# Optimization experiments

Hardware: AMD Instinct MI355X
Metric: run time of the kernel (lower is better)

The kernel has to match this reference:

```python
import jax, jax.numpy as jnp
import numpy as np

N = 256
MAX_LENGTH = 1024
BATCH = 32768


def _transition(n):
    # HiPPO-LegS transition matrices (float64 numpy, matches torch module)
    q = np.arange(n, dtype=np.float64)
    col, row = np.meshgrid(q, q)
    r = 2 * q + 1
    M = -(np.where(row >= col, r, 0) - np.diag(q))
    T = np.sqrt(np.diag(2 * q + 1))
    A = T @ M @ np.linalg.inv(T)
    B = np.diag(T)  # squeezed (N,)
    return A, B


def _build_stacked(n, max_length):
    # Bilinear (Tustin) discretization at every timescale t=1..max_length.
    A, B = _transition(n)
    ts = np.arange(1, max_length + 1, dtype=np.float64)  # (L,)
    At = A[None] / ts[:, None, None]                     # (L,N,N)
    Bt = B[None] / ts[:, None]                           # (L,N)
    I = np.eye(n)
    lhs = I[None] - At / 2                               # (L,N,N), lower triangular
    A_stacked = np.linalg.solve(lhs, I[None] + At / 2)   # (L,N,N)
    B_stacked = np.linalg.solve(lhs, Bt[..., None])[..., 0]  # (L,N)
    return A_stacked.astype(np.float32), B_stacked.astype(np.float32)


def setup_inputs() -> dict:
    key = jax.random.key(0)
    k1, k2 = jax.random.split(key)
    A_np, B_np = _build_stacked(N, MAX_LENGTH)
    return {
        "c": jax.random.normal(k1, (BATCH, N), dtype=jnp.float32),
        "f": jax.random.normal(k2, (BATCH, 1), dtype=jnp.float32),
        "A_stacked": jnp.asarray(A_np),  # (L, N, N) buffer
        "B_stacked": jnp.asarray(B_np),  # (L, N) buffer
        "t": 512,
    }


def reference(c, f, A_stacked, B_stacked, t):
    # F.linear(c, A) == c @ A.T ; then scaled add of new value f
    A = A_stacked[t]            # (N, N)
    b = B_stacked[t]            # (N,)
    return c @ A.T + b * f      # (BATCH, N)
```

## Files before the change

### kernel.cpp

```cpp
#include <hip/hip_runtime.h>
#include <cstdint>
#include <cstddef>

typedef _Float16 half8 __attribute__((ext_vector_type(8)));
typedef float f32x4 __attribute__((ext_vector_type(4)));

static constexpr int kN  = 256;
static constexpr int kKS = 8;
static constexpr size_t kABytes = (size_t)kN * kN * 2;

__global__ __launch_bounds__(256) void hippo_prep(
    const float* __restrict__ A_stacked, const int* __restrict__ tptr,
    _Float16* __restrict__ a16)
{
    const int t = tptr[0];
    const float* __restrict__ A = A_stacked + (size_t)t * kN * kN;
    const int tid = blockIdx.x * 256 + threadIdx.x;
    const int nt = tid >> 9;
    const int ks = (tid >> 6) & 7;
    const int l  = tid & 63;
    const int row = nt * 16 + (l & 15);
    const int k0  = ks * 32 + ((l >> 4) << 3);
    const float* __restrict__ src = A + row * kN + k0;
    f32x4 v0 = *(const f32x4*)(src);
    f32x4 v1 = *(const f32x4*)(src + 4);
    half8 h;
    h[0] = (_Float16)v0[0]; h[1] = (_Float16)v0[1];
    h[2] = (_Float16)v0[2]; h[3] = (_Float16)v0[3];
    h[4] = (_Float16)v1[0]; h[5] = (_Float16)v1[1];
    h[6] = (_Float16)v1[2]; h[7] = (_Float16)v1[3];
    ((half8*)a16)[tid] = h;
}

__global__ __launch_bounds__(512, 2) void hippo_gemm(
    const float* __restrict__ c, const float* __restrict__ f,
    const float* __restrict__ Bst, const int* __restrict__ tptr,
    const _Float16* __restrict__ a16, float* __restrict__ out)
{
    extern __shared__ char lds_raw[];

    const int tid  = threadIdx.x;
    const int l    = tid & 63;
    const int wid  = tid >> 6;
    const int wm   = wid & 3;
    const int wn   = wid >> 2;
    const int lo16 = l & 15;
    const int hi4  = l >> 4;
    const int m0   = blockIdx.x * 128 + wm * 16;
    const int m1   = m0 + 64;
    const int ntb  = wn * 8;

    const float* __restrict__ cp0 = c + (size_t)(m0 + lo16) * kN + (hi4 << 3);
    f32x4 cv0[kKS], cv1[kKS];
    #pragma unroll
    for (int ks = 0; ks < kKS; ++ks) {
        cv0[ks] = *(const f32x4*)(cp0 + ks * 32);
        cv1[ks] = *(const f32x4*)(cp0 + ks * 32 + 4);
    }

    #pragma unroll
    for (int i = 0; i < 16; ++i) {
        const size_t off = (size_t)(i * 8 + wid) * 1024 + (size_t)l * 16;
        __builtin_amdgcn_global_load_lds(
            (const __attribute__((address_space(1))) void*)((const char*)a16 + off),
            (__attribute__((address_space(3))) void*)(lds_raw + off),
            16, 0, 0);
    }

    const int t = tptr[0];
    const float* __restrict__ brow = Bst + (size_t)t * kN + wn * 128;
    float bvs[8];
    #pragma unroll
    for (int nt = 0; nt < 8; ++nt) bvs[nt] = brow[nt * 16 + lo16];
    float fv0[4], fv1[4];
    #pragma unroll
    for (int r = 0; r < 4; ++r) {
        fv0[r] = f[m0 + (hi4 << 2) + r];
        fv1[r] = f[m1 + (hi4 << 2) + r];
    }

    __syncthreads();

    const float* __restrict__ cp1 = c + (size_t)(m1 + lo16) * kN + (hi4 << 3);
    f32x4 dv0[kKS], dv1[kKS];
    #pragma unroll
    for (int ks = 0; ks < kKS; ++ks) {
        dv0[ks] = *(const f32x4*)(cp1 + ks * 32);
        dv1[ks] = *(const f32x4*)(cp1 + ks * 32 + 4);
    }

    half8 af[kKS];
    #pragma unroll
    for (int ks = 0; ks < kKS; ++ks) {
        af[ks][0] = (_Float16)cv0[ks][0]; af[ks][1] = (_Float16)cv0[ks][1];
        af[ks][2] = (_Float16)cv0[ks][2]; af[ks][3] = (_Float16)cv0[ks][3];
        af[ks][4] = (_Float16)cv1[ks][0]; af[ks][5] = (_Float16)cv1[ks][1];
        af[ks][6] = (_Float16)cv1[ks][2]; af[ks][7] = (_Float16)cv1[ks][3];
    }
    const half8* __restrict__ Bs = (const half8*)lds_raw;
    f32x4 acc[8];
    #pragma unroll
    for (int i = 0; i < 8; ++i) acc[i] = (f32x4){0.f, 0.f, 0.f, 0.f};
    #pragma unroll
    for (int ks = 0; ks < kKS; ++ks) {
        #pragma unroll
        for (int nt = 0; nt < 8; ++nt) {
            half8 bf = Bs[((ntb + nt) * kKS + ks) * 64 + l];
            acc[nt] = __builtin_amdgcn_mfma_f32_16x16x32_f16(af[ks], bf, acc[nt], 0, 0, 0);
        }
    }
    float* __restrict__ ob0 = out + (size_t)(m0 + (hi4 << 2)) * kN + wn * 128 + lo16;
    #pragma unroll
    for (int nt = 0; nt < 8; ++nt) {
        #pragma unroll
        for (int r = 0; r < 4; ++r)
            ob0[(size_t)r * kN + nt * 16] = acc[nt][r] + bvs[nt] * fv0[r];
    }

    half8 ag[kKS];
    #pragma unroll
    for (int ks = 0; ks < kKS; ++ks) {
        ag[ks][0] = (_Float16)dv0[ks][0]; ag[ks][1] = (_Float16)dv0[ks][1];
        ag[ks][2] = (_Float16)dv0[ks][2]; ag[ks][3] = (_Float16)dv0[ks][3];
        ag[ks][4] = (_Float16)dv1[ks][0]; ag[ks][5] = (_Float16)dv1[ks][1];
        ag[ks][6] = (_Float16)dv1[ks][2]; ag[ks][7] = (_Float16)dv1[ks][3];
    }
    f32x4 acc2[8];
    #pragma unroll
    for (int i = 0; i < 8; ++i) acc2[i] = (f32x4){0.f, 0.f, 0.f, 0.f};
    #pragma unroll
    for (int ks = 0; ks < kKS; ++ks) {
        #pragma unroll
        for (int nt = 0; nt < 8; ++nt) {
            half8 bf = Bs[((ntb + nt) * kKS + ks) * 64 + l];
            acc2[nt] = __builtin_amdgcn_mfma_f32_16x16x32_f16(ag[ks], bf, acc2[nt], 0, 0, 0);
        }
    }
    float* __restrict__ ob1 = out + (size_t)(m1 + (hi4 << 2)) * kN + wn * 128 + lo16;
    #pragma unroll
    for (int nt = 0; nt < 8; ++nt) {
        #pragma unroll
        for (int r = 0; r < 4; ++r)
            ob1[(size_t)r * kN + nt * 16] = acc2[nt][r] + bvs[nt] * fv1[r];
    }
}

extern "C" void kernel_launch(void* const* d_in, const int* in_sizes, int n_in,
                              void* d_out, int out_size, void* d_ws, size_t ws_size,
                              hipStream_t stream) {
    const float* c   = (const float*)d_in[0];
    const float* f   = (const float*)d_in[1];
    const float* A   = (const float*)d_in[2];
    const float* B   = (const float*)d_in[3];
    const int*   t   = (const int*)d_in[4];
    float* out = (float*)d_out;
    _Float16* a16 = (_Float16*)d_ws;

    const int batch = in_sizes[0] / kN;

    hipFuncSetAttribute((const void*)hippo_gemm,
                        hipFuncAttributeMaxDynamicSharedMemorySize,
                        (int)kABytes);

    hipLaunchKernelGGL(hippo_prep, dim3(32), dim3(256), 0, stream, A, t, a16);
    hipLaunchKernelGGL(hippo_gemm, dim3(batch / 128), dim3(512), kABytes, stream,
                       c, f, B, t, a16, out);
}
```

Measured before the change: 25.82 us.

## Hoist second row-tile loads before barrier and interleave both MFMA chains per N-tile

Both 64-row halves of the c tile are now loaded from global memory before the LDS barrier rather than after it. The loop order is also restructured: for each N-tile, one LDS B fragment is read once and fed to two MFMA accumulator chains, one per row half, and both outputs are written right away. This halves LDS reads of the A matrix and gives two independent MFMA dependency chains, and it issues all global loads earlier to hide latency. The cost is more registers live at once, since 32 f32x4 loads are in flight before the barrier, which could hurt occupancy under the 2-blocks-per-CU launch bound.

```diff
diff --git a/kernel.cpp b/kernel.cpp
--- a/kernel.cpp
+++ b/kernel.cpp
@@ -51,11 +51,14 @@
     const int ntb  = wn * 8;
 
     const float* __restrict__ cp0 = c + (size_t)(m0 + lo16) * kN + (hi4 << 3);
-    f32x4 cv0[kKS], cv1[kKS];
+    const float* __restrict__ cp1 = cp0 + (size_t)64 * kN;
+    f32x4 cv0[kKS], cv1[kKS], dv0[kKS], dv1[kKS];
     #pragma unroll
     for (int ks = 0; ks < kKS; ++ks) {
         cv0[ks] = *(const f32x4*)(cp0 + ks * 32);
         cv1[ks] = *(const f32x4*)(cp0 + ks * 32 + 4);
+        dv0[ks] = *(const f32x4*)(cp1 + ks * 32);
+        dv1[ks] = *(const f32x4*)(cp1 + ks * 32 + 4);
     }
 
     #pragma unroll
@@ -81,67 +84,38 @@
 
     __syncthreads();
 
-    const float* __restrict__ cp1 = c + (size_t)(m1 + lo16) * kN + (hi4 << 3);
-    f32x4 dv0[kKS], dv1[kKS];
-    #pragma unroll
-    for (int ks = 0; ks < kKS; ++ks) {
-        dv0[ks] = *(const f32x4*)(cp1 + ks * 32);
-        dv1[ks] = *(const f32x4*)(cp1 + ks * 32 + 4);
-    }
-
-    half8 af[kKS];
+    half8 af[kKS], ag[kKS];
     #pragma unroll
     for (int ks = 0; ks < kKS; ++ks) {
         af[ks][0] = (_Float16)cv0[ks][0]; af[ks][1] = (_Float16)cv0[ks][1];
         af[ks][2] = (_Float16)cv0[ks][2]; af[ks][3] = (_Float16)cv0[ks][3];
         af[ks][4] = (_Float16)cv1[ks][0]; af[ks][5] = (_Float16)cv1[ks][1];
         af[ks][6] = (_Float16)cv1[ks][2]; af[ks][7] = (_Float16)cv1[ks][3];
-    }
-    const half8* __restrict__ Bs = (const half8*)lds_raw;
-    f32x4 acc[8];
-    #pragma unroll
-    for (int i = 0; i < 8; ++i) acc[i] = (f32x4){0.f, 0.f, 0.f, 0.f};
-    #pragma unroll
-    for (int ks = 0; ks < kKS; ++ks) {
-        #pragma unroll
-        for (int nt = 0; nt < 8; ++nt) {
-            half8 bf = Bs[((ntb + nt) * kKS + ks) * 64 + l];
-            acc[nt] = __builtin_amdgcn_mfma_f32_16x16x32_f16(af[ks], bf, acc[nt], 0, 0, 0);
-        }
-    }
-    float* __restrict__ ob0 = out + (size_t)(m0 + (hi4 << 2)) * kN + wn * 128 + lo16;
-    #pragma unroll
-    for (int nt = 0; nt < 8; ++nt) {
-        #pragma unroll
-        for (int r = 0; r < 4; ++r)
-            ob0[(size_t)r * kN + nt * 16] = acc[nt][r] + bvs[nt] * fv0[r];
-    }
-
-    half8 ag[kKS];
-    #pragma unroll
-    for (int ks = 0; ks < kKS; ++ks) {
         ag[ks][0] = (_Float16)dv0[ks][0]; ag[ks][1] = (_Float16)dv0[ks][1];
         ag[ks][2] = (_Float16)dv0[ks][2]; ag[ks][3] = (_Float16)dv0[ks][3];
         ag[ks][4] = (_Float16)dv1[ks][0]; ag[ks][5] = (_Float16)dv1[ks][1];
         ag[ks][6] = (_Float16)dv1[ks][2]; ag[ks][7] = (_Float16)dv1[ks][3];
     }
-    f32x4 acc2[8];
-    #pragma unroll
-    for (int i = 0; i < 8; ++i) acc2[i] = (f32x4){0.f, 0.f, 0.f, 0.f};
-    #pragma unroll
-    for (int ks = 0; ks < kKS; ++ks) {
-        #pragma unroll
-        for (int nt = 0; nt < 8; ++nt) {
-            half8 bf = Bs[((ntb + nt) * kKS + ks) * 64 + l];
-            acc2[nt] = __builtin_amdgcn_mfma_f32_16x16x32_f16(ag[ks], bf, acc2[nt], 0, 0, 0);
-        }
-    }
-    float* __restrict__ ob1 = out + (size_t)(m1 + (hi4 << 2)) * kN + wn * 128 + lo16;
+
+    const half8* __restrict__ Bs = (const half8*)lds_raw;
+    float* __restrict__ ob0 = out + (size_t)(m0 + (hi4 << 2)) * kN + wn * 128 + lo16;
+    float* __restrict__ ob1 = ob0 + (size_t)64 * kN;
+
     #pragma unroll
     for (int nt = 0; nt < 8; ++nt) {
+        f32x4 acc0 = (f32x4){0.f, 0.f, 0.f, 0.f};
+        f32x4 acc1 = (f32x4){0.f, 0.f, 0.f, 0.f};
         #pragma unroll
-        for (int r = 0; r < 4; ++r)
-            ob1[(size_t)r * kN + nt * 16] = acc2[nt][r] + bvs[nt] * fv1[r];
+        for (int ks = 0; ks < kKS; ++ks) {
+            half8 bf = Bs[((ntb + nt) * kKS + ks) * 64 + l];
+            acc0 = __builtin_amdgcn_mfma_f32_16x16x32_f16(af[ks], bf, acc0, 0, 0, 0);
+            acc1 = __builtin_amdgcn_mfma_f32_16x16x32_f16(ag[ks], bf, acc1, 0, 0, 0);
+        }
+        #pragma unroll
+        for (int r = 0; r < 4; ++r) {
+            ob0[(size_t)r * kN + nt * 16] = acc0[r] + bvs[nt] * fv0[r];
+            ob1[(size_t)r * kN + nt * 16] = acc1[r] + bvs[nt] * fv1[r];
+        }
     }
 }
 
```

Measured after the change: 27.89 us. 1.08x slower.
